# Kernel optimization log

Measured on AMD Instinct MI355X. Metric: run time of the kernel, lower is better.

## Reference

```python
import jax, jax.numpy as jnp
import numpy as np

TEMP = 0.07
EPS = 1e-6

B = 8192
D1 = 129  # d+1 ambient Lorentz coords


def setup_inputs() -> dict:
    key = jax.random.key(0)
    k1, k2 = jax.random.split(key)
    z1 = jax.random.normal(k1, (B, D1), dtype=jnp.float32)
    z2 = jax.random.normal(k2, (B, D1), dtype=jnp.float32)
    return {"z1": z1, "z2": z2}


def _loss(z1, z2):
    # Minkowski (Lorentz) inner product via a single GEMM:
    # <x,y>_L = -x0*y0 + sum_i xi*yi  ->  x @ (metric * y)^T
    metric = jnp.concatenate([-jnp.ones((1,), z1.dtype), jnp.ones((D1 - 1,), z1.dtype)])
    inner = jnp.einsum('bd,kd->bk', z1, z2 * metric)  # (B, B)
    # Lorentz distance with curvature c=1: acosh(clamp(-<x,y>_L, 1+eps))
    dist = jnp.arccosh(jnp.clip(-inner, 1.0 + EPS, None))
    sims = -dist / TEMP
    # symmetric InfoNCE: labels are the diagonal
    logp_t2i = jax.nn.log_softmax(sims, axis=-1)      # text -> image
    logp_i2t = jax.nn.log_softmax(sims.T, axis=-1)    # image -> text
    diag = jnp.arange(sims.shape[0])
    loss_t2i = -jnp.mean(logp_t2i[diag, diag])
    loss_i2t = -jnp.mean(logp_i2t[diag, diag])
    return (loss_t2i + loss_i2t) / 2.0


def reference(z1, z2):
    return _loss(z1, z2)
```

## Files before the change

### kernel.cpp

```cpp
#include <hip/hip_runtime.h>
#include <math.h>


#define BDIM   8192
#define K_IN   129
#define K_PAD  160
#define BK     32
#define NKT    5
#define CTILES 8

typedef __bf16  bf16x8 __attribute__((ext_vector_type(8)));
typedef float   f32x4  __attribute__((ext_vector_type(4)));
typedef unsigned short u16x4 __attribute__((ext_vector_type(4)));

#define OFF_A    0u
#define OFF_B    (BDIM * K_PAD * 2u)
#define OFF_RS   (2u * BDIM * K_PAD * 2u)
#define OFF_CP   (OFF_RS + BDIM * 4u)
#define OFF_DG   (OFF_CP + 4u * BDIM * 4u)

__device__ __forceinline__ float fast_sqrt(float x) {
#if __has_builtin(__builtin_amdgcn_sqrtf)
    return __builtin_amdgcn_sqrtf(x);
#else
    return sqrtf(x);
#endif
}
__device__ __forceinline__ float fast_log2(float x) {
#if __has_builtin(__builtin_amdgcn_logf)
    return __builtin_amdgcn_logf(x);
#else
    return __log2f(x);
#endif
}
__device__ __forceinline__ float fast_exp2(float x) {
#if __has_builtin(__builtin_amdgcn_exp2f)
    return __builtin_amdgcn_exp2f(x);
#else
    extern "C" __device__ float __ocml_native_exp2_f32(float);
    return __ocml_native_exp2_f32(x);
#endif
}

__device__ __forceinline__ unsigned short f2bf_rne(float f) {
    unsigned int u = __float_as_uint(f);
    u += 0x7FFFu + ((u >> 16) & 1u);
    return (unsigned short)(u >> 16);
}

__global__ __launch_bounds__(256) void convert_kernel(
    const float* __restrict__ z1, const float* __restrict__ z2,
    unsigned short* __restrict__ A, unsigned short* __restrict__ B,
    float* __restrict__ rs_cp)
{
    int v = blockIdx.x * 256 + threadIdx.x;
    if (v < 5 * BDIM) rs_cp[v] = 0.f;
    if (v >= BDIM * (K_PAD / 4)) return;
    int r  = v / (K_PAD / 4);
    int c4 = (v - r * (K_PAD / 4)) * 4;
    u16x4 a, b;
    #pragma unroll
    for (int i = 0; i < 4; ++i) {
        int c = c4 + i;
        float va = 0.f, vb = 0.f;
        if (c < K_IN) {
            va = z1[r * K_IN + c];
            vb = z2[r * K_IN + c];
            if (c == 0) va = -va;
        }
        a[i] = f2bf_rne(va);
        b[i] = f2bf_rne(vb);
    }
    *(u16x4*)(A + r * K_PAD + c4) = a;
    *(u16x4*)(B + r * K_PAD + c4) = b;
}


#define STAGE(bufidx, cb)                                                     \
    {                                                                         \
        const char* _gp = (const char*)(B + (size_t)(cb) * K_PAD)             \
                          + wave * 5120 + lane * 16;                          \
        unsigned short* _lp = &Bs[bufidx][wave * 2560];                       \
        _Pragma("unroll")                                                     \
        for (int _i = 0; _i < 5; ++_i)                                        \
            __builtin_amdgcn_global_load_lds(                                 \
                (const __attribute__((address_space(1))) void*)               \
                    (_gp + _i * 1024),                                        \
                (__attribute__((address_space(3))) void*)(_lp + _i * 512),    \
                16, 0, 0);                                                    \
    }

#define COMPUTE(bufidx, cb)                                                   \
    {                                                                         \
        const int colBase = (cb);                                             \
        const unsigned short* _Bt = &Bs[bufidx][0];                           \
        f32x4 acc[2][4] = {};                                                 \
        _Pragma("unroll")                                                     \
        for (int kt = 0; kt < NKT; ++kt) {                                    \
            bf16x8 bfr[4];                                                    \
            _Pragma("unroll")                                                 \
            for (int j = 0; j < 4; ++j)                                       \
                bfr[j] = *(const bf16x8*)                                     \
                    &_Bt[(l16 + j * 16) * K_PAD + quad * 8 + kt * BK];        \
            _Pragma("unroll")                                                 \
            for (int i = 0; i < 2; ++i)                                       \
                _Pragma("unroll")                                             \
                for (int j = 0; j < 4; ++j)                                   \
                    acc[i][j] = __builtin_amdgcn_mfma_f32_16x16x32_bf16(      \
                        Ah[i][kt], bfr[j], acc[i][j], 0, 0, 0);               \
        }                                                                     \
        const bool diagTile = (colBase == (rowBase & ~63));                   \
        const int  dj       = (rowBase >> 4) & 2;                             \
        float colp[4] = {0.f, 0.f, 0.f, 0.f};                                 \
        _Pragma("unroll")                                                     \
        for (int i = 0; i < 2; ++i) {                                         \
            _Pragma("unroll")                                                 \
            for (int j = 0; j < 4; ++j) {                                     \
                _Pragma("unroll")                                             \
                for (int reg = 0; reg < 4; ++reg) {                           \
                    float inner = acc[i][j][reg];                             \
                    float x = fmaxf(-inner, 1.000001f);                       \
                    float s = fast_sqrt(__builtin_fmaf(x, x, -1.0f));         \
                    float l2u = fast_log2(x + s);                             \
                    float e = fast_exp2(-14.285714285714286f * l2u);          \
                    rowp[i][reg] += e;                                        \
                    colp[j]      += e;                                        \
                    if (diagTile && (j - i) == dj && (quad * 4 + reg) == l16){\
                        int R = rowBase + i * 16 + quad * 4 + reg;            \
                        diag[R] = -9.902102579427789f * l2u;                  \
                    }                                                         \
                }                                                             \
            }                                                                 \
        }                                                                     \
        _Pragma("unroll")                                                     \
        for (int j = 0; j < 4; ++j) {                                         \
            float v = colp[j];                                                \
            v += __shfl_xor(v, 16);                                           \
            v += __shfl_xor(v, 32);                                           \
            if (quad == 0)                                                    \
                atomicAdd(&colRep[colBase + j * 16 + l16], v);                \
        }                                                                     \
    }

__global__ __launch_bounds__(256, 4) void gemm_epilogue_kernel(
    const unsigned short* __restrict__ A, const unsigned short* __restrict__ B,
    float* __restrict__ row_sum, float* __restrict__ col_part,
    float* __restrict__ diag)
{
    const int t    = threadIdx.x;
    const int lane = t & 63;
    const int wave = t >> 6;
    const int quad = lane >> 4;
    const int l16  = lane & 15;

    const int strip = blockIdx.x & 63;
    const int chunk = blockIdx.x >> 6;
    const int rowBase  = strip * 128 + wave * 32;
    const int colChunk = chunk * 512;

    const unsigned short* Abase = A + (rowBase + l16) * K_PAD + quad * 8;
    float* colRep = col_part + (strip & 3) * BDIM;

    __shared__ __align__(16) unsigned short Bs[2][64 * K_PAD];

    bf16x8 Ah[2][NKT];
    #pragma unroll
    for (int i = 0; i < 2; ++i)
        #pragma unroll
        for (int kt = 0; kt < NKT; ++kt)
            Ah[i][kt] = *(const bf16x8*)(Abase + i * 16 * K_PAD + kt * BK);

    float rowp[2][4] = {};

    STAGE(0, colChunk);
    __syncthreads();

    #pragma unroll 1
    for (int ct = 0; ct < CTILES; ++ct) {
        if (ct + 1 < CTILES)
            STAGE((ct + 1) & 1, colChunk + (ct + 1) * 64);
        COMPUTE(ct & 1, colChunk + ct * 64);
        __syncthreads();
    }

    #pragma unroll
    for (int i = 0; i < 2; ++i) {
        #pragma unroll
        for (int reg = 0; reg < 4; ++reg) {
            float v = rowp[i][reg];
            v += __shfl_xor(v, 1);
            v += __shfl_xor(v, 2);
            v += __shfl_xor(v, 4);
            v += __shfl_xor(v, 8);
            if (l16 == 0)
                atomicAdd(&row_sum[rowBase + i * 16 + quad * 4 + reg], v);
        }
    }
}

__global__ __launch_bounds__(1024) void finalize_kernel(
    const float* __restrict__ rs, const float* __restrict__ cp,
    const float* __restrict__ dg, float* __restrict__ out)
{
    __shared__ float part[16];
    int t = threadIdx.x;
    float a = 0.f;
    const float LN2_HALF = 0.34657359027997264f;
    for (int b = t; b < BDIM; b += 1024) {
        float cs = cp[b] + cp[b + BDIM] + cp[b + 2 * BDIM] + cp[b + 3 * BDIM];
        a += LN2_HALF * (fast_log2(rs[b]) + fast_log2(cs)) - dg[b];
    }
    #pragma unroll
    for (int m = 1; m < 64; m <<= 1) a += __shfl_xor(a, m);
    if ((t & 63) == 0) part[t >> 6] = a;
    __syncthreads();
    if (t < 16) {
        float v = part[t];
        #pragma unroll
        for (int m = 1; m < 16; m <<= 1) v += __shfl_xor(v, m);
        if (t == 0) out[0] = v * (1.0f / (float)BDIM);
    }
}

extern "C" void kernel_launch(void* const* d_in, const int* in_sizes, int n_in,
                              void* d_out, int out_size, void* d_ws, size_t ws_size,
                              hipStream_t stream)
{
    const float* z1 = (const float*)d_in[0];
    const float* z2 = (const float*)d_in[1];
    float* out = (float*)d_out;

    char* ws = (char*)d_ws;
    unsigned short* A  = (unsigned short*)(ws + OFF_A);
    unsigned short* B  = (unsigned short*)(ws + OFF_B);
    float* row_sum     = (float*)(ws + OFF_RS);
    float* col_part    = (float*)(ws + OFF_CP);
    float* diag        = (float*)(ws + OFF_DG);

    convert_kernel<<<(BDIM * (K_PAD / 4) + 255) / 256, 256, 0, stream>>>(
        z1, z2, A, B, row_sum );

    gemm_epilogue_kernel<<<1024, 256, 0, stream>>>(
        A, B, row_sum, col_part, diag);

    finalize_kernel<<<1, 1024, 0, stream>>>(row_sum, col_part, diag, out);
}
```

Before: 108.8 us.

## Give each wave its own 16-column B tile pipeline and drop block barriers

Each wave now stages its own 16-column slice of B into a private double-buffered LDS region with direct global-to-LDS loads. It waits on its own loads through `s_waitcnt vmcnt`, so the per-tile `__syncthreads` is gone. The loop runs 32 phases of 16 columns instead of 8 phases of 64, so each phase issues fewer MFMAs and does fewer column atomics. The aim is to let waves run the heavy transcendental epilogue out of lockstep and overlap loads without block-wide stalls. In exchange, the four waves of a block each fetch the same B data, which multiplies load traffic, and there is less independent MFMA work per phase to hide latency.

```diff
diff --git a/kernel.cpp b/kernel.cpp
--- a/kernel.cpp
+++ b/kernel.cpp
@@ -7,7 +7,7 @@
 #define K_PAD  160
 #define BK     32
 #define NKT    5
-#define CTILES 8
+#define NPH    32
 
 typedef __bf16  bf16x8 __attribute__((ext_vector_type(8)));
 typedef float   f32x4  __attribute__((ext_vector_type(4)));
@@ -76,70 +76,58 @@
 }
 
 
-#define STAGE(bufidx, cb)                                                     \
+#define STAGE16(bufidx, cb)                                                   \
     {                                                                         \
         const char* _gp = (const char*)(B + (size_t)(cb) * K_PAD)             \
-                          + wave * 5120 + lane * 16;                          \
-        unsigned short* _lp = &Bs[bufidx][wave * 2560];                       \
+                          + lane * 16;                                        \
+        char* _lp = (char*)&Bs[wave][bufidx][0];                              \
         _Pragma("unroll")                                                     \
-        for (int _i = 0; _i < 5; ++_i)                                        \
+        for (int _m = 0; _m < 5; ++_m)                                        \
             __builtin_amdgcn_global_load_lds(                                 \
                 (const __attribute__((address_space(1))) void*)               \
-                    (_gp + _i * 1024),                                        \
-                (__attribute__((address_space(3))) void*)(_lp + _i * 512),    \
+                    (_gp + _m * 1024),                                        \
+                (__attribute__((address_space(3))) void*)(_lp + _m * 1024),   \
                 16, 0, 0);                                                    \
     }
 
-#define COMPUTE(bufidx, cb)                                                   \
+#define COMPUTE16(bufidx, cb)                                                 \
     {                                                                         \
         const int colBase = (cb);                                             \
-        const unsigned short* _Bt = &Bs[bufidx][0];                           \
-        f32x4 acc[2][4] = {};                                                 \
+        const unsigned short* _Bt = &Bs[wave][bufidx][0];                     \
+        f32x4 acc[2] = {};                                                    \
         _Pragma("unroll")                                                     \
         for (int kt = 0; kt < NKT; ++kt) {                                    \
-            bf16x8 bfr[4];                                                    \
-            _Pragma("unroll")                                                 \
-            for (int j = 0; j < 4; ++j)                                       \
-                bfr[j] = *(const bf16x8*)                                     \
-                    &_Bt[(l16 + j * 16) * K_PAD + quad * 8 + kt * BK];        \
-            _Pragma("unroll")                                                 \
-            for (int i = 0; i < 2; ++i)                                       \
-                _Pragma("unroll")                                             \
-                for (int j = 0; j < 4; ++j)                                   \
-                    acc[i][j] = __builtin_amdgcn_mfma_f32_16x16x32_bf16(      \
-                        Ah[i][kt], bfr[j], acc[i][j], 0, 0, 0);               \
+            bf16x8 bfr = *(const bf16x8*)                                     \
+                &_Bt[l16 * K_PAD + quad * 8 + kt * BK];                       \
+            acc[0] = __builtin_amdgcn_mfma_f32_16x16x32_bf16(                 \
+                         Ah[0][kt], bfr, acc[0], 0, 0, 0);                    \
+            acc[1] = __builtin_amdgcn_mfma_f32_16x16x32_bf16(                 \
+                         Ah[1][kt], bfr, acc[1], 0, 0, 0);                    \
         }                                                                     \
-        const bool diagTile = (colBase == (rowBase & ~63));                   \
-        const int  dj       = (rowBase >> 4) & 2;                             \
-        float colp[4] = {0.f, 0.f, 0.f, 0.f};                                 \
+        float colp = 0.f;                                                     \
         _Pragma("unroll")                                                     \
         for (int i = 0; i < 2; ++i) {                                         \
+            const bool diagTile = (colBase == rowBase + i * 16);              \
             _Pragma("unroll")                                                 \
-            for (int j = 0; j < 4; ++j) {                                     \
-                _Pragma("unroll")                                             \
-                for (int reg = 0; reg < 4; ++reg) {                           \
-                    float inner = acc[i][j][reg];                             \
-                    float x = fmaxf(-inner, 1.000001f);                       \
-                    float s = fast_sqrt(__builtin_fmaf(x, x, -1.0f));         \
-                    float l2u = fast_log2(x + s);                             \
-                    float e = fast_exp2(-14.285714285714286f * l2u);          \
-                    rowp[i][reg] += e;                                        \
-                    colp[j]      += e;                                        \
-                    if (diagTile && (j - i) == dj && (quad * 4 + reg) == l16){\
-                        int R = rowBase + i * 16 + quad * 4 + reg;            \
-                        diag[R] = -9.902102579427789f * l2u;                  \
-                    }                                                         \
+            for (int reg = 0; reg < 4; ++reg) {                               \
+                float inner = acc[i][reg];                                    \
+                float x = fmaxf(-inner, 1.000001f);                           \
+                float s = fast_sqrt(__builtin_fmaf(x, x, -1.0f));             \
+                float l2u = fast_log2(x + s);                                 \
+                float e = fast_exp2(-14.285714285714286f * l2u);              \
+                rowp[i][reg] += e;                                            \
+                colp         += e;                                            \
+                if (diagTile && (quad * 4 + reg) == l16) {                    \
+                    int R = rowBase + i * 16 + quad * 4 + reg;                \
+                    diag[R] = -9.902102579427789f * l2u;                      \
                 }                                                             \
             }                                                                 \
         }                                                                     \
-        _Pragma("unroll")                                                     \
-        for (int j = 0; j < 4; ++j) {                                         \
-            float v = colp[j];                                                \
-            v += __shfl_xor(v, 16);                                           \
-            v += __shfl_xor(v, 32);                                           \
-            if (quad == 0)                                                    \
-                atomicAdd(&colRep[colBase + j * 16 + l16], v);                \
-        }                                                                     \
+        float v = colp;                                                       \
+        v += __shfl_xor(v, 16);                                               \
+        v += __shfl_xor(v, 32);                                               \
+        if (quad == 0)                                                        \
+            atomicAdd(&colRep[colBase + l16], v);                             \
     }
 
 __global__ __launch_bounds__(256, 4) void gemm_epilogue_kernel(
@@ -161,7 +149,7 @@
     const unsigned short* Abase = A + (rowBase + l16) * K_PAD + quad * 8;
     float* colRep = col_part + (strip & 3) * BDIM;
 
-    __shared__ __align__(16) unsigned short Bs[2][64 * K_PAD];
+    __shared__ __align__(16) unsigned short Bs[4][2][16 * K_PAD];
 
     bf16x8 Ah[2][NKT];
     #pragma unroll
@@ -172,15 +160,18 @@
 
     float rowp[2][4] = {};
 
-    STAGE(0, colChunk);
-    __syncthreads();
+    STAGE16(0, colChunk);
 
     #pragma unroll 1
-    for (int ct = 0; ct < CTILES; ++ct) {
-        if (ct + 1 < CTILES)
-            STAGE((ct + 1) & 1, colChunk + (ct + 1) * 64);
-        COMPUTE(ct & 1, colChunk + ct * 64);
-        __syncthreads();
+    for (int ct = 0; ct < NPH; ++ct) {
+        if (ct + 1 < NPH) {
+            STAGE16((ct + 1) & 1, colChunk + (ct + 1) * 16);
+            asm volatile("s_waitcnt vmcnt(5)" ::: "memory");
+        } else {
+            asm volatile("s_waitcnt vmcnt(0)" ::: "memory");
+        }
+        __builtin_amdgcn_sched_barrier(0);
+        COMPUTE16(ct & 1, colChunk + ct * 16);
     }
 
     #pragma unroll
```

After: 117.5 us. 8.0% more time.

## Replace global atomics with per-block partial sums and parallel finalize

Applied to the files above, without the earlier changes.

Column partial sums are now gathered per wave in shared memory and written non-atomically to a per-strip buffer, and row sums go to per-chunk slots, so the global atomicAdds and the zeroing pass in the convert kernel are gone. The finalize kernel becomes a 64-block reduction over these partial buffers and combines its results with one atomic add into a memset output. This removes atomic contention but adds workspace traffic (64 column partials per element), an extra memset, and more shared memory per block, which may lower occupancy.

```diff
diff --git a/kernel.cpp b/kernel.cpp
--- a/kernel.cpp
+++ b/kernel.cpp
@@ -8,16 +8,18 @@
 #define BK     32
 #define NKT    5
 #define CTILES 8
+#define NCHUNK 16
+#define NSTRIP 64
 
 typedef __bf16  bf16x8 __attribute__((ext_vector_type(8)));
 typedef float   f32x4  __attribute__((ext_vector_type(4)));
 typedef unsigned short u16x4 __attribute__((ext_vector_type(4)));
 
-#define OFF_A    0u
-#define OFF_B    (BDIM * K_PAD * 2u)
-#define OFF_RS   (2u * BDIM * K_PAD * 2u)
-#define OFF_CP   (OFF_RS + BDIM * 4u)
-#define OFF_DG   (OFF_CP + 4u * BDIM * 4u)
+#define OFF_A     0u
+#define OFF_B     (BDIM * K_PAD * 2u)
+#define OFF_RP    (2u * BDIM * K_PAD * 2u)
+#define OFF_CPART (OFF_RP + NCHUNK * BDIM * 4u)
+#define OFF_DG    (OFF_CPART + NSTRIP * BDIM * 4u)
 
 __device__ __forceinline__ float fast_sqrt(float x) {
 #if __has_builtin(__builtin_amdgcn_sqrtf)
@@ -50,11 +52,9 @@
 
 __global__ __launch_bounds__(256) void convert_kernel(
     const float* __restrict__ z1, const float* __restrict__ z2,
-    unsigned short* __restrict__ A, unsigned short* __restrict__ B,
-    float* __restrict__ rs_cp)
+    unsigned short* __restrict__ A, unsigned short* __restrict__ B)
 {
     int v = blockIdx.x * 256 + threadIdx.x;
-    if (v < 5 * BDIM) rs_cp[v] = 0.f;
     if (v >= BDIM * (K_PAD / 4)) return;
     int r  = v / (K_PAD / 4);
     int c4 = (v - r * (K_PAD / 4)) * 4;
@@ -137,14 +137,16 @@
             float v = colp[j];                                                \
             v += __shfl_xor(v, 16);                                           \
             v += __shfl_xor(v, 32);                                           \
-            if (quad == 0)                                                    \
-                atomicAdd(&colRep[colBase + j * 16 + l16], v);                \
+            if (quad == 0) {                                                  \
+                int _ci = wave * 512 + (colBase - colChunk) + j * 16 + l16;   \
+                colAcc[_ci] += v;       \
+            }                                                                 \
         }                                                                     \
     }
 
 __global__ __launch_bounds__(256, 4) void gemm_epilogue_kernel(
     const unsigned short* __restrict__ A, const unsigned short* __restrict__ B,
-    float* __restrict__ row_sum, float* __restrict__ col_part,
+    float* __restrict__ rp, float* __restrict__ cpart,
     float* __restrict__ diag)
 {
     const int t    = threadIdx.x;
@@ -159,9 +161,12 @@
     const int colChunk = chunk * 512;
 
     const unsigned short* Abase = A + (rowBase + l16) * K_PAD + quad * 8;
-    float* colRep = col_part + (strip & 3) * BDIM;
 
     __shared__ __align__(16) unsigned short Bs[2][64 * K_PAD];
+    __shared__ float colAcc[4 * 512];
+
+    #pragma unroll
+    for (int c = t; c < 4 * 512; c += 256) colAcc[c] = 0.f;
 
     bf16x8 Ah[2][NKT];
     #pragma unroll
@@ -193,33 +198,40 @@
             v += __shfl_xor(v, 4);
             v += __shfl_xor(v, 8);
             if (l16 == 0)
-                atomicAdd(&row_sum[rowBase + i * 16 + quad * 4 + reg], v);
+                rp[chunk * BDIM + rowBase + i * 16 + quad * 4 + reg] = v;
         }
     }
-}
-
-__global__ __launch_bounds__(1024) void finalize_kernel(
-    const float* __restrict__ rs, const float* __restrict__ cp,
+    __syncthreads();
+    for (int c = t; c < 512; c += 256) {
+        float s = colAcc[c] + colAcc[512 + c] + colAcc[1024 + c] +
+                  colAcc[1536 + c];
+        cpart[strip * BDIM + colChunk + c] = s;
+    }
+}
+
+__global__ __launch_bounds__(256) void finalize_kernel(
+    const float* __restrict__ rp, const float* __restrict__ cpart,
     const float* __restrict__ dg, float* __restrict__ out)
 {
-    __shared__ float part[16];
+    __shared__ float part[2];
     int t = threadIdx.x;
     float a = 0.f;
     const float LN2_HALF = 0.34657359027997264f;
-    for (int b = t; b < BDIM; b += 1024) {
-        float cs = cp[b] + cp[b + BDIM] + cp[b + 2 * BDIM] + cp[b + 3 * BDIM];
-        a += LN2_HALF * (fast_log2(rs[b]) + fast_log2(cs)) - dg[b];
+    if (t < 128) {
+        int b = blockIdx.x * 128 + t;
+        float rs = 0.f, cs = 0.f;
+        #pragma unroll
+        for (int c = 0; c < NCHUNK; ++c) rs += rp[c * BDIM + b];
+        #pragma unroll
+        for (int s = 0; s < NSTRIP; ++s) cs += cpart[s * BDIM + b];
+        a = LN2_HALF * (fast_log2(rs) + fast_log2(cs)) - dg[b];
     }
     #pragma unroll
     for (int m = 1; m < 64; m <<= 1) a += __shfl_xor(a, m);
-    if ((t & 63) == 0) part[t >> 6] = a;
+    if ((t & 63) == 0 && t < 128) part[t >> 6] = a;
     __syncthreads();
-    if (t < 16) {
-        float v = part[t];
-        #pragma unroll
-        for (int m = 1; m < 16; m <<= 1) v += __shfl_xor(v, m);
-        if (t == 0) out[0] = v * (1.0f / (float)BDIM);
-    }
+    if (t == 0)
+        atomicAdd(out, (part[0] + part[1]) * (1.0f / (float)BDIM));
 }
 
 extern "C" void kernel_launch(void* const* d_in, const int* in_sizes, int n_in,
@@ -233,15 +245,17 @@
     char* ws = (char*)d_ws;
     unsigned short* A  = (unsigned short*)(ws + OFF_A);
     unsigned short* B  = (unsigned short*)(ws + OFF_B);
-    float* row_sum     = (float*)(ws + OFF_RS);
-    float* col_part    = (float*)(ws + OFF_CP);
+    float* rp          = (float*)(ws + OFF_RP);
+    float* cpart       = (float*)(ws + OFF_CPART);
     float* diag        = (float*)(ws + OFF_DG);
 
+    hipMemsetAsync(out, 0, sizeof(float), stream);
+
     convert_kernel<<<(BDIM * (K_PAD / 4) + 255) / 256, 256, 0, stream>>>(
-        z1, z2, A, B, row_sum );
+        z1, z2, A, B);
 
     gemm_epilogue_kernel<<<1024, 256, 0, stream>>>(
-        A, B, row_sum, col_part, diag);
-
-    finalize_kernel<<<1, 1024, 0, stream>>>(row_sum, col_part, diag, out);
-}
+        A, B, rp, cpart, diag);
+
+    finalize_kernel<<<NSTRIP, 256, 0, stream>>>(rp, cpart, diag, out);
+}
```

Result: slower. 131.9 us (+21.3%).
